# Performance work log

Measured on AMD Instinct MI355X. Metric: run time of the kernel, lower is better.

The kernel has to match this reference:

```python
import jax, jax.numpy as jnp
import numpy as np

V, E, H, L = 32000, 512, 1024, 2
B, T, S = 32, 64, 64


def setup_inputs() -> dict:
    key = jax.random.key(0)
    ks = jax.random.split(key, 20)
    sc = 0.05
    return {
        "tgt_seq": jax.random.randint(ks[0], (B, T), 0, V),
        "encoder_outputs": jax.random.normal(ks[1], (B, S, H), jnp.float32),
        "h0": jax.random.normal(ks[2], (L, B, H), jnp.float32) * sc,
        "c0": jax.random.normal(ks[3], (L, B, H), jnp.float32) * sc,
        "mask": jnp.ones((B, S), dtype=bool),
        "emb": jax.random.normal(ks[4], (V, E), jnp.float32) * sc,
        "W1": jax.random.normal(ks[5], (H, H), jnp.float32) * sc,
        "b1": jnp.zeros((H,), jnp.float32),
        "W2": jax.random.normal(ks[6], (H, H), jnp.float32) * sc,
        "b2": jnp.zeros((H,), jnp.float32),
        "v": jax.random.normal(ks[7], (H,), jnp.float32) * sc,
        "bv": jnp.zeros((), jnp.float32),
        "W_ih0": jax.random.normal(ks[8], (4 * H, E + H), jnp.float32) * sc,
        "W_hh0": jax.random.normal(ks[9], (4 * H, H), jnp.float32) * sc,
        "b_ih0": jnp.zeros((4 * H,), jnp.float32),
        "b_hh0": jnp.zeros((4 * H,), jnp.float32),
        "W_ih1": jax.random.normal(ks[10], (4 * H, H), jnp.float32) * sc,
        "W_hh1": jax.random.normal(ks[11], (4 * H, H), jnp.float32) * sc,
        "b_ih1": jnp.zeros((4 * H,), jnp.float32),
        "b_hh1": jnp.zeros((4 * H,), jnp.float32),
    }


def _lstm_cell(x, h, c, W_ih, W_hh, b_ih, b_hh):
    gates = x @ W_ih.T + b_ih + h @ W_hh.T + b_hh  # [B, 4H]
    i, f, g, o = jnp.split(gates, 4, axis=-1)      # torch gate order i,f,g,o
    c_new = jax.nn.sigmoid(f) * c + jax.nn.sigmoid(i) * jnp.tanh(g)
    h_new = jax.nn.sigmoid(o) * jnp.tanh(c_new)
    return h_new, c_new


def reference(tgt_seq, encoder_outputs, h0, c0, mask, emb, W1, b1, W2, b2, v, bv,
              W_ih0, W_hh0, b_ih0, b_hh0, W_ih1, W_hh1, b_ih1, b_hh1):
    embedded = emb[tgt_seq]                       # [B, T, E] (eval mode: dropout no-op)
    # Encoder projection for Bahdanau attention is time-invariant: precompute.
    enc_proj = encoder_outputs @ W2.T + b2        # [B, S, H]
    layer_params = [(W_ih0, W_hh0, b_ih0, b_hh0), (W_ih1, W_hh1, b_ih1, b_hh1)]

    def step(carry, emb_t):
        h, c = carry                              # each [L, B, H]
        dec_h = h[-1]                             # top-layer hidden, [B, H]
        # Bahdanau: score = v . tanh(W1 h + W2 enc)
        e = jnp.tanh((dec_h @ W1.T + b1)[:, None, :] + enc_proj)  # [B, S, H]
        scores = e @ v + bv                       # [B, S]
        scores = jnp.where(mask, scores, -1e9)
        attn = jax.nn.softmax(scores, axis=-1)
        ctx = jnp.einsum('bs,bsh->bh', attn, encoder_outputs)     # [B, H]
        x = jnp.concatenate([emb_t, ctx], axis=-1)                # [B, E+H]
        new_h, new_c = [], []
        for l in range(L):
            hl, cl = _lstm_cell(x, h[l], c[l], *layer_params[l])
            new_h.append(hl); new_c.append(cl)
            x = hl
        return (jnp.stack(new_h), jnp.stack(new_c)), x            # x = top-layer output

    (h_n, c_n), outs = jax.lax.scan(step, (h0, c0), jnp.swapaxes(embedded, 0, 1))
    decoder_outputs = jnp.swapaxes(outs, 0, 1)    # [B, T, H]
    return decoder_outputs, (h_n, c_n)
```

## Files before the change

kernel.cpp:

```cpp
#include <hip/hip_runtime.h>
#include <hip/hip_bf16.h>

#define NB 32
#define NT 64
#define NS 64
#define NH 1024
#define NE 512
#define NG 4096
#define NWG 256

typedef __attribute__((ext_vector_type(8))) short bf16x8;
typedef __attribute__((ext_vector_type(4))) float f32x4;
typedef __hip_bfloat16 bf16;

#define MFMA(a,b,c) __builtin_amdgcn_mfma_f32_16x16x32_bf16((a),(b),(c),0,0,0)

__device__ __align__(16) bf16 g_W1b  [NH*NH];
__device__ __align__(16) bf16 g_W2b  [NH*NH];
__device__ __align__(16) bf16 g_Whh0b[NG*NH];
__device__ __align__(16) bf16 g_Wih0cb[NG*NH];
__device__ __align__(16) bf16 g_Wih0eb[NG*NE];
__device__ __align__(16) bf16 g_Wih1b[NG*NH];
__device__ __align__(16) bf16 g_Whh1b[NG*NH];
__device__ __align__(16) bf16 g_encb [NB*NS*NH];
__device__ __align__(16) bf16 g_encpb[NB*NS*NH];
__device__ __align__(16) bf16 g_embtb[NT*NB*NE];
__device__ __align__(16) float g_preemb[NT*NB*NG];
__device__ __align__(16) float g_b1s[NG];
__device__ __align__(16) bf16 g_encWr[NWG*512*64];
__device__ __align__(16) bf16 g_h0buf[(NT+1)*NB*NH];
__device__ __align__(16) bf16 g_h1buf[(NT+1)*NB*NH];
__device__ __align__(16) float g_scores[NT*NB*NS];
__device__ int g_fsc[64];
__device__ int g_fh0[256];
__device__ int g_fh1[256];

__device__ __forceinline__ void st_f32(float* p, float v) {
  __hip_atomic_store(p, v, __ATOMIC_RELAXED, __HIP_MEMORY_SCOPE_AGENT);
}
__device__ __forceinline__ void st_u32(unsigned* p, unsigned v) {
  __hip_atomic_store(p, v, __ATOMIC_RELAXED, __HIP_MEMORY_SCOPE_AGENT);
}
__device__ __forceinline__ void st_i32(int* p, int v) {
  __hip_atomic_store(p, v, __ATOMIC_RELAXED, __HIP_MEMORY_SCOPE_AGENT);
}
__device__ __forceinline__ int ld_i32(const int* p) {
  return __hip_atomic_load(p, __ATOMIC_RELAXED, __HIP_MEMORY_SCOPE_AGENT);
}
__device__ __forceinline__ float ld_f32(const float* p) {
  return __hip_atomic_load(p, __ATOMIC_RELAXED, __HIP_MEMORY_SCOPE_AGENT);
}
__device__ __forceinline__ void at_addf(float* p, float v) {
  __hip_atomic_fetch_add(p, v, __ATOMIC_RELAXED, __HIP_MEMORY_SCOPE_AGENT);
}
__device__ __forceinline__ unsigned short f2bf_u(float x) {
  bf16 h = __float2bfloat16(x);
  unsigned short u; __builtin_memcpy(&u, &h, 2); return u;
}
__device__ __forceinline__ float sigm(float x)   { return 1.f / (1.f + __expf(-x)); }
__device__ __forceinline__ float tanh_f(float x) { return 1.f - 2.f / (1.f + __expf(2.f * x)); }
__device__ __forceinline__ float bf2f(short u) {
  return __uint_as_float(((unsigned)(unsigned short)u) << 16);
}

__device__ __forceinline__ void wait_flags256(const int* f, int tgt) {
  if (threadIdx.x < 64) {
    const int base = threadIdx.x * 4;
    for (;;) {
      int a = ld_i32(f + base),     b = ld_i32(f + base + 1);
      int c = ld_i32(f + base + 2), d = ld_i32(f + base + 3);
      if (__all(a >= tgt && b >= tgt && c >= tgt && d >= tgt)) break;
      __builtin_amdgcn_s_sleep(1);
    }
  }
  asm volatile("" ::: "memory");
  __syncthreads();
}
__device__ __forceinline__ void wait_flags64(const int* f, int tgt) {
  if (threadIdx.x < 64) {
    for (;;) {
      if (__all(ld_i32(f + threadIdx.x) >= tgt)) break;
      __builtin_amdgcn_s_sleep(2);
    }
  }
  asm volatile("" ::: "memory");
  __syncthreads();
}

__device__ __forceinline__ f32x4 gemm16h_lds_pf(const bf16* __restrict__ A, const bf16* Bsw,
                                                int l15, int kf8, int kh) {
  bf16x8 a[16];
  const bf16* ar = A + (size_t)l15*NH + kh*512 + kf8*8;
  #pragma unroll
  for (int k = 0; k < 16; ++k) a[k] = *(const bf16x8*)(ar + k*32);
  f32x4 acc = {0,0,0,0};
  #pragma unroll
  for (int k = 0; k < 16; ++k) {
    int bg = kh*64 + k*4 + kf8;
    acc = MFMA(a[k], *(const bf16x8*)(Bsw + (l15*128 + ((bg & ~7) | ((bg & 7) ^ (l15 & 7))))*8), acc);
  }
  return acc;
}
__device__ __forceinline__ void gemm16h_dual_pf(const bf16* __restrict__ A, const bf16* B0,
                                                const bf16* B1, int l15, int kf8, int kh,
                                                f32x4* o0, f32x4* o1) {
  bf16x8 a[16];
  const bf16* ar = A + (size_t)l15*NH + kh*512 + kf8*8;
  #pragma unroll
  for (int k = 0; k < 16; ++k) a[k] = *(const bf16x8*)(ar + k*32);
  f32x4 u = {0,0,0,0}, w = {0,0,0,0};
  #pragma unroll
  for (int k = 0; k < 16; ++k) {
    int bg = kh*64 + k*4 + kf8;
    int of = (l15*128 + ((bg & ~7) | ((bg & 7) ^ (l15 & 7))))*8;
    u = MFMA(a[k], *(const bf16x8*)(B0 + of), u);
    w = MFMA(a[k], *(const bf16x8*)(B1 + of), w);
  }
  *o0 = u; *o1 = w;
}

__global__ __launch_bounds__(256) void prep(const float* W1, const float* W2, const float* Whh0,
    const float* Wih0, const float* Wih1, const float* Whh1, const float* enc,
    const float* emb, const int* tgt) {
  long i = (long)blockIdx.x * 256 + threadIdx.x;
  if (i < 1048576) { g_W1b[i] = __float2bfloat16(W1[i]); return; } i -= 1048576;
  if (i < 1048576) { g_W2b[i] = __float2bfloat16(W2[i]); return; } i -= 1048576;
  if (i < 4194304) { g_Whh0b[i] = __float2bfloat16(Whh0[i]); return; } i -= 4194304;
  if (i < 4194304) { long r = i >> 10, c = i & 1023;
                     g_Wih0cb[i] = __float2bfloat16(Wih0[r*1536 + 512 + c]); return; } i -= 4194304;
  if (i < 2097152) { long r = i >> 9, c = i & 511;
                     g_Wih0eb[i] = __float2bfloat16(Wih0[r*1536 + c]); return; } i -= 2097152;
  if (i < 4194304) { g_Wih1b[i] = __float2bfloat16(Wih1[i]); return; } i -= 4194304;
  if (i < 4194304) { g_Whh1b[i] = __float2bfloat16(Whh1[i]); return; } i -= 4194304;
  if (i < 2097152) { g_encb[i] = __float2bfloat16(enc[i]); return; } i -= 2097152;
  { long e = i & 511, tb = i >> 9, tt = tb >> 5, b = tb & 31;
    g_embtb[i] = __float2bfloat16(emb[(long)tgt[b*NT + tt]*NE + e]); }
}

__global__ __launch_bounds__(256) void init_state(const float* h0in, const float* bih1,
                                                  const float* bhh1) {
  int i = blockIdx.x * 256 + threadIdx.x;
  if (i < NB*NH) {
    g_h0buf[i] = __float2bfloat16(h0in[i]);
    g_h1buf[i] = __float2bfloat16(h0in[NB*NH + i]);
  }
  if (i < NG) g_b1s[i] = bih1[i] + bhh1[i];
  st_f32(&g_scores[2*i], 0.f);
  st_f32(&g_scores[2*i + 1], 0.f);
  if (i < 256) { st_i32(&g_fh0[i], 0); st_i32(&g_fh1[i], 0); }
  if (i < 64) st_i32(&g_fsc[i], 0);
}

__device__ void gemm32(const bf16* __restrict__ A, const bf16* __restrict__ Bw,
                       const float* bias0, const float* bias1,
                       bf16* outB, float* outF, int M, int N, int K) {
  int gw = blockIdx.x * 4 + (threadIdx.x >> 6);
  int lane = threadIdx.x & 63;
  int nb = N >> 5;
  int mi = gw / nb, ni = gw - mi * nb;
  if (mi >= (M >> 5)) return;
  int l15 = lane & 15, lk = (lane >> 4) * 8;
  f32x4 acc00 = {0,0,0,0}, acc01 = {0,0,0,0}, acc10 = {0,0,0,0}, acc11 = {0,0,0,0};
  const bf16* a0p = A  + (size_t)(mi*32 + l15)*K + lk;
  const bf16* a1p = a0p + (size_t)16*K;
  const bf16* b0p = Bw + (size_t)(ni*32 + l15)*K + lk;
  const bf16* b1p = b0p + (size_t)16*K;
  for (int k = 0; k < K; k += 32) {
    bf16x8 a0 = *(const bf16x8*)(a0p + k);
    bf16x8 a1 = *(const bf16x8*)(a1p + k);
    bf16x8 b0 = *(const bf16x8*)(b0p + k);
    bf16x8 b1 = *(const bf16x8*)(b1p + k);
    acc00 = MFMA(a0, b0, acc00); acc01 = MFMA(a0, b1, acc01);
    acc10 = MFMA(a1, b0, acc10); acc11 = MFMA(a1, b1, acc11);
  }
  int r0 = (lane >> 4) * 4;
  #pragma unroll
  for (int nt = 0; nt < 2; ++nt) {
    int col = ni*32 + nt*16 + l15;
    float bs = (bias0 ? bias0[col] : 0.f) + (bias1 ? bias1[col] : 0.f);
    f32x4 s0 = nt ? acc01 : acc00;
    f32x4 s1 = nt ? acc11 : acc10;
    #pragma unroll
    for (int r = 0; r < 4; ++r) {
      int row0 = mi*32 + r0 + r, row1 = row0 + 16;
      float v0 = s0[r] + bs, v1 = s1[r] + bs;
      if (outB) { outB[(size_t)row0*N + col] = __float2bfloat16(v0);
                  outB[(size_t)row1*N + col] = __float2bfloat16(v1); }
      else      { outF[(size_t)row0*N + col] = v0;
                  outF[(size_t)row1*N + col] = v1; }
    }
  }
}
__global__ __launch_bounds__(256) void k_encproj(const float* b2) {
  gemm32(g_encb, g_W2b, b2, nullptr, g_encpb, nullptr, NB*NS, NH, NH);
}
__global__ __launch_bounds__(256) void k_preemb(const float* bih0, const float* bhh0) {
  gemm32(g_embtb, g_Wih0eb, bih0, bhh0, nullptr, g_preemb, NT*NB, NG, NE);
}
__global__ __launch_bounds__(256) void k_encw() {
  int gw = blockIdx.x * 4 + (threadIdx.x >> 6);
  int lane = threadIdx.x & 63;
  int mi = gw >> 7, ni = gw & 127;
  int l15 = lane & 15, lk = (lane >> 4) * 8;
  f32x4 acc00 = {0,0,0,0}, acc01 = {0,0,0,0}, acc10 = {0,0,0,0}, acc11 = {0,0,0,0};
  const bf16* a0p = g_encb + (size_t)(mi*32 + l15)*NH + lk;
  const bf16* a1p = a0p + (size_t)16*NH;
  const bf16* b0p = g_Wih0cb + (size_t)(ni*32 + l15)*NH + lk;
  const bf16* b1p = b0p + (size_t)16*NH;
  for (int k = 0; k < NH; k += 32) {
    bf16x8 a0 = *(const bf16x8*)(a0p + k);
    bf16x8 a1 = *(const bf16x8*)(a1p + k);
    bf16x8 b0 = *(const bf16x8*)(b0p + k);
    bf16x8 b1 = *(const bf16x8*)(b1p + k);
    acc00 = MFMA(a0, b0, acc00); acc01 = MFMA(a0, b1, acc01);
    acc10 = MFMA(a1, b0, acc10); acc11 = MFMA(a1, b1, acc11);
  }
  int r0 = (lane >> 4) * 4;
  #pragma unroll
  for (int nt = 0; nt < 2; ++nt) {
    int col = ni*32 + nt*16 + l15;
    int ow = (col & 1023) >> 2, lgc = ((col >> 10) << 2) | (col & 3);
    f32x4 s0 = nt ? acc01 : acc00;
    f32x4 s1 = nt ? acc11 : acc10;
    #pragma unroll
    for (int r = 0; r < 4; ++r) {
      int row0 = mi*32 + r0 + r, row1 = row0 + 16;
      int b0r = row0 >> 6, s0r = row0 & 63, b1r = row1 >> 6, s1r = row1 & 63;
      g_encWr[(((size_t)ow*32 + b0r)*16 + lgc)*64 + s0r] = __float2bfloat16(s0[r]);
      g_encWr[(((size_t)ow*32 + b1r)*16 + lgc)*64 + s1r] = __float2bfloat16(s1[r]);
    }
  }
}

__global__ __launch_bounds__(256, 1) void dec_loop(const float* __restrict__ b1,
    const float* __restrict__ v, const float* __restrict__ c0, float* __restrict__ out) {
  const int wg = blockIdx.x, tid = threadIdx.x;
  const int lane = tid & 63, wv = tid >> 6;
  const int l15 = lane & 15, kf8 = lane >> 4;
  const int mt = wv & 1, kh = wv >> 1;
  const int pr = mt*16 + kf8*4;

  __shared__ __align__(16) bf16 sw[4][16*1024];
  __shared__ float s_tmp[1024];
  __shared__ float sg0p[2][512];
  __shared__ float sg1p[512];
  __shared__ float s_dp[512];
  __shared__ float sattn[NB*64];
  __shared__ float gatesF[512];
  __shared__ float scst[2][128];

  #pragma unroll
  for (int q = 0; q < 24; ++q) {
    int gi = q*256 + tid;
    int g = gi >> 11, rem = gi & 2047;
    int gc = rem >> 7, gk = rem & 127;
    int gate = gc >> 2, hc = gc & 3;
    const bf16* src = (g == 0) ? g_Whh0b : (g == 1) ? g_Whh1b : g_Wih1b;
    bf16x8 w8 = *(const bf16x8*)(src + (size_t)(gate*NH + wg*4 + hc)*NH + gk*8);
    int gks = (gk & ~7) | ((gk & 7) ^ (gc & 7));
    *(bf16x8*)(&sw[g][(gc*128 + gks)*8]) = w8;
  }
  const bool is_dp = (wg >= 64 && wg < 128);
  const int  u = wg - 64;
  if (is_dp) {
    #pragma unroll
    for (int q = 0; q < 8; ++q) {
      int gi = q*256 + tid, gc = gi >> 7, gk = gi & 127;
      bf16x8 w8 = *(const bf16x8*)(g_W1b + (size_t)(u*16 + gc)*NH + gk*8);
      int gks = (gk & ~7) | ((gk & 7) ^ (gc & 7));
      *(bf16x8*)(&sw[3][(gc*128 + gks)*8]) = w8;
    }
  }
  if (tid < 128) {
    scst[0][tid] = c0[(size_t)(tid >> 2)*NH + wg*4 + (tid & 3)];
    scst[1][tid] = c0[(size_t)(NB + (tid >> 2))*NH + wg*4 + (tid & 3)];
  }
  __syncthreads();

  bf16x8 w0[8], w1[8];
  {
    const bf16* e0 = g_encWr + ((size_t)wg*512 + tid)*64;
    const bf16* e1 = g_encWr + ((size_t)wg*512 + 256 + tid)*64;
    #pragma unroll
    for (int i = 0; i < 8; ++i) w0[i] = *(const bf16x8*)(e0 + i*8);
    #pragma unroll
    for (int i = 0; i < 8; ++i) w1[i] = *(const bf16x8*)(e1 + i*8);
  }

  const int  gcolr = ((tid & 15) >> 2)*NH + wg*4 + (tid & 3);
  const float b1s_r = g_b1s[gcolr];
  const float dpb = is_dp ? b1[u*16 + (tid & 15)] : 0.f;
  float vr[16];
  if (is_dp) {
    #pragma unroll
    for (int c = 0; c < 16; ++c) vr[c] = v[u*16 + c];
  }
  float* out_hn = out + (size_t)NB*NT*NH;
  float* out_cn = out_hn + 2*NB*NH;

  {
    f32x4 acc = gemm16h_lds_pf(g_h0buf + (size_t)mt*16*NH, sw[0], l15, kf8, kh);
    #pragma unroll
    for (int r = 0; r < 4; ++r) sg0p[kh][(pr + r)*16 + l15] = acc[r];
  }

  for (int t = 0; t < NT; ++t) {
    const float* pe = g_preemb + (size_t)t*NB*NG;
    float pe0 = pe[(size_t)(tid >> 4)*NG + gcolr];
    float pe1 = pe[(size_t)(16 + (tid >> 4))*NG + gcolr];

    wait_flags256(g_fh1, t);
    const bf16* h1t = g_h1buf + (size_t)t*NB*NH;

    if (is_dp) {
      f32x4 aD = gemm16h_lds_pf(h1t + (size_t)mt*16*NH, sw[3], l15, kf8, kh);
      #pragma unroll
      for (int r = 0; r < 4; ++r) s_tmp[kh*512 + (pr + r)*16 + l15] = aD[r];
      __syncthreads();
      s_dp[tid]       = s_tmp[tid]       + s_tmp[512 + tid]       + dpb;
      s_dp[256 + tid] = s_tmp[256 + tid] + s_tmp[768 + tid]       + dpb;
      __syncthreads();
      {
        const int bb = tid >> 3, s0 = (tid & 7)*8;
        float dpr[16];
        #pragma unroll
        for (int c = 0; c < 16; ++c) dpr[c] = s_dp[bb*16 + c];
        #pragma unroll
        for (int k = 0; k < 8; ++k) {
          int s = s0 + ((k + u) & 7);
          const bf16* ep = g_encpb + ((size_t)(bb*NS + s))*NH + u*16;
          bf16x8 ea = *(const bf16x8*)ep;
          bf16x8 eb = *(const bf16x8*)(ep + 8);
          float p = 0.f;
          #pragma unroll
          for (int c = 0; c < 8; ++c) p += vr[c]     * tanh_f(dpr[c]     + bf2f(ea[c]));
          #pragma unroll
          for (int c = 0; c < 8; ++c) p += vr[8 + c] * tanh_f(dpr[8 + c] + bf2f(eb[c]));
          at_addf(&g_scores[(size_t)t*2048 + bb*64 + s], p);
        }
      }
      __syncthreads();
      if (tid == 0) st_i32(&g_fsc[u], t + 1);
    }

    if (wv < 2) {
      f32x4 x0 = gemm16h_lds_pf(h1t + (size_t)wv*16*NH, sw[1], l15, kf8, 0);
      f32x4 x1 = gemm16h_lds_pf(h1t + (size_t)wv*16*NH, sw[1], l15, kf8, 1);
      x0 += x1;
      #pragma unroll
      for (int r = 0; r < 4; ++r) sg1p[(wv*16 + kf8*4 + r)*16 + l15] = x0[r];
    }

    wait_flags64(g_fsc, t + 1);
    {
      const int bb = tid >> 3, s0 = (tid & 7)*8;
      float sc[8];
      #pragma unroll
      for (int k = 0; k < 8; ++k) sc[k] = ld_f32(&g_scores[(size_t)t*2048 + bb*64 + s0 + k]);
      float m = sc[0];
      #pragma unroll
      for (int k = 1; k < 8; ++k) m = fmaxf(m, sc[k]);
      #pragma unroll
      for (int o = 1; o < 8; o <<= 1) m = fmaxf(m, __shfl_xor(m, o, 64));
      float S = 0.f, e8[8];
      #pragma unroll
      for (int k = 0; k < 8; ++k) { e8[k] = __expf(sc[k] - m); S += e8[k]; }
      #pragma unroll
      for (int o = 1; o < 8; o <<= 1) S += __shfl_xor(S, o, 64);
      float invS = 1.f / S;
      #pragma unroll
      for (int k = 0; k < 8; ++k) sattn[bb*64 + s0 + k] = e8[k] * invS;
    }
    __syncthreads();
    {
      const float* at0 = sattn + (tid >> 4)*64;
      const float* at1 = sattn + (16 + (tid >> 4))*64;
      float acc0 = 0.f, acc1 = 0.f;
      #pragma unroll
      for (int i = 0; i < 8; ++i) {
        #pragma unroll
        for (int j = 0; j < 8; ++j) {
          acc0 += at0[i*8 + j] * bf2f(w0[i][j]);
          acc1 += at1[i*8 + j] * bf2f(w1[i][j]);
        }
      }
      gatesF[tid]       = acc0 + sg0p[0][tid]       + sg0p[1][tid]       + pe0;
      gatesF[256 + tid] = acc1 + sg0p[0][256 + tid] + sg0p[1][256 + tid] + pe1;
    }
    __syncthreads();
    if (tid < 128) {
      int b = tid >> 2, hc = tid & 3, col = wg*4 + hc;
      float Gi = gatesF[b*16 + hc],     Gf = gatesF[b*16 + 4 + hc];
      float Gg = gatesF[b*16 + 8 + hc], Go = gatesF[b*16 + 12 + hc];
      float ii = sigm(Gi), ff = sigm(Gf), gg = tanh_f(Gg), oo = sigm(Go);
      float c = scst[0][tid], cn = ff*c + ii*gg;
      float hn = oo * tanh_f(cn);
      scst[0][tid] = cn;
      unsigned hu = f2bf_u(hn);
      unsigned ho = __shfl_down(hu, 1, 64);
      if ((tid & 1) == 0)
        st_u32((unsigned*)(g_h0buf + (size_t)(t+1)*NB*NH + (size_t)b*NH + col), hu | (ho << 16));
      if (t == NT - 1) { out_hn[(size_t)b*NH + col] = hn; out_cn[(size_t)b*NH + col] = cn; }
    }
    __syncthreads();
    if (tid == 0) st_i32(&g_fh0[wg], t + 1);

    wait_flags256(g_fh0, t + 1);
    {
      const bf16* h0t1 = g_h0buf + (size_t)(t+1)*NB*NH;
      f32x4 aU, aV;
      gemm16h_dual_pf(h0t1 + (size_t)mt*16*NH, sw[2], sw[0], l15, kf8, kh, &aU, &aV);
      #pragma unroll
      for (int r = 0; r < 4; ++r) {
        s_tmp[kh*512 + (pr + r)*16 + l15] = aU[r];
        sg0p[kh][(pr + r)*16 + l15]       = aV[r];
      }
      __syncthreads();
      gatesF[tid]       = s_tmp[tid]       + s_tmp[512 + tid] + sg1p[tid]       + b1s_r;
      gatesF[256 + tid] = s_tmp[256 + tid] + s_tmp[768 + tid] + sg1p[256 + tid] + b1s_r;
      __syncthreads();
      if (tid < 128) {
        int b = tid >> 2, hc = tid & 3, col = wg*4 + hc;
        float Gi = gatesF[b*16 + hc],     Gf = gatesF[b*16 + 4 + hc];
        float Gg = gatesF[b*16 + 8 + hc], Go = gatesF[b*16 + 12 + hc];
        float ii = sigm(Gi), ff = sigm(Gf), gg = tanh_f(Gg), oo = sigm(Go);
        float c = scst[1][tid], cn = ff*c + ii*gg;
        float hn = oo * tanh_f(cn);
        scst[1][tid] = cn;
        unsigned hu = f2bf_u(hn);
        unsigned ho = __shfl_down(hu, 1, 64);
        if ((tid & 1) == 0)
          st_u32((unsigned*)(g_h1buf + (size_t)(t+1)*NB*NH + (size_t)b*NH + col), hu | (ho << 16));
        out[((size_t)b*NT + t)*NH + col] = hn;
        if (t == NT - 1) { out_hn[(size_t)(NB + b)*NH + col] = hn; out_cn[(size_t)(NB + b)*NH + col] = cn; }
      }
      __syncthreads();
      if (tid == 0) st_i32(&g_fh1[wg], t + 1);
    }
  }
}

extern "C" void kernel_launch(void* const* d_in, const int* in_sizes, int n_in,
                              void* d_out, int out_size, void* d_ws, size_t ws_size,
                              hipStream_t stream) {
  (void)in_sizes; (void)n_in; (void)d_ws; (void)ws_size; (void)out_size;
  const int*   tgt  = (const int*)  d_in[0];
  const float* enc  = (const float*)d_in[1];
  const float* h0   = (const float*)d_in[2];
  const float* c0   = (const float*)d_in[3];
  const float* emb  = (const float*)d_in[5];
  const float* W1   = (const float*)d_in[6];
  const float* b1   = (const float*)d_in[7];
  const float* W2   = (const float*)d_in[8];
  const float* b2   = (const float*)d_in[9];
  const float* v    = (const float*)d_in[10];
  const float* Wih0 = (const float*)d_in[12];
  const float* Whh0 = (const float*)d_in[13];
  const float* bih0 = (const float*)d_in[14];
  const float* bhh0 = (const float*)d_in[15];
  const float* Wih1 = (const float*)d_in[16];
  const float* Whh1 = (const float*)d_in[17];
  const float* bih1 = (const float*)d_in[18];
  const float* bhh1 = (const float*)d_in[19];
  float* out = (float*)d_out;

  prep<<<dim3(94208), dim3(256), 0, stream>>>(W1, W2, Whh0, Wih0, Wih1, Whh1, enc, emb, tgt);
  init_state<<<dim3(256), dim3(256), 0, stream>>>(h0, bih1, bhh1);
  k_encproj<<<dim3(512), dim3(256), 0, stream>>>(b2);
  k_preemb<<<dim3(2048), dim3(256), 0, stream>>>(bih0, bhh0);
  k_encw<<<dim3(2048), dim3(256), 0, stream>>>();
  dec_loop<<<dim3(NWG), dim3(256), 0, stream>>>(b1, v, c0, out);
}
```

Before: 2.347 ms.

## Split batch into two chunks with per-chunk flags to pipeline decoder stages

The persistent decoder loop now handles the batch as two 16-row chunks, each with its own set of global progress flags for scores, layer-0 and layer-1 hidden states. Workgroups can start a later stage on chunk 0 while other workgroups are still finishing chunk 1, which is meant to hide grid-wide barrier latency. Each warp now covers a K-quarter of a 16-row tile instead of a half of a 32-row tile, and the score wait sleeps for a shorter time. The cost is twice as many flag waits and syncthreads per step, plus a four-way reduction of partial sums through LDS.

```diff
diff --git a/kernel.cpp b/kernel.cpp
--- a/kernel.cpp
+++ b/kernel.cpp
@@ -2,6 +2,7 @@
 #include <hip/hip_bf16.h>
 
 #define NB 32
+#define NBC 16
 #define NT 64
 #define NS 64
 #define NH 1024
@@ -31,9 +32,9 @@
 __device__ __align__(16) bf16 g_h0buf[(NT+1)*NB*NH];
 __device__ __align__(16) bf16 g_h1buf[(NT+1)*NB*NH];
 __device__ __align__(16) float g_scores[NT*NB*NS];
-__device__ int g_fsc[64];
-__device__ int g_fh0[256];
-__device__ int g_fh1[256];
+__device__ int g_fsc[2][64];
+__device__ int g_fh0[2][256];
+__device__ int g_fh1[2][256];
 
 __device__ __forceinline__ void st_f32(float* p, float v) {
   __hip_atomic_store(p, v, __ATOMIC_RELAXED, __HIP_MEMORY_SCOPE_AGENT);
@@ -80,38 +81,38 @@
   if (threadIdx.x < 64) {
     for (;;) {
       if (__all(ld_i32(f + threadIdx.x) >= tgt)) break;
-      __builtin_amdgcn_s_sleep(2);
+      __builtin_amdgcn_s_sleep(1);
     }
   }
   asm volatile("" ::: "memory");
   __syncthreads();
 }
 
-__device__ __forceinline__ f32x4 gemm16h_lds_pf(const bf16* __restrict__ A, const bf16* Bsw,
-                                                int l15, int kf8, int kh) {
-  bf16x8 a[16];
-  const bf16* ar = A + (size_t)l15*NH + kh*512 + kf8*8;
-  #pragma unroll
-  for (int k = 0; k < 16; ++k) a[k] = *(const bf16x8*)(ar + k*32);
+__device__ __forceinline__ f32x4 gemm16q_pf(const bf16* __restrict__ A, const bf16* Bsw,
+                                            int l15, int kf8, int kq) {
+  bf16x8 a[8];
+  const bf16* ar = A + (size_t)l15*NH + kq*256 + kf8*8;
+  #pragma unroll
+  for (int k = 0; k < 8; ++k) a[k] = *(const bf16x8*)(ar + k*32);
   f32x4 acc = {0,0,0,0};
   #pragma unroll
-  for (int k = 0; k < 16; ++k) {
-    int bg = kh*64 + k*4 + kf8;
+  for (int k = 0; k < 8; ++k) {
+    int bg = kq*32 + k*4 + kf8;
     acc = MFMA(a[k], *(const bf16x8*)(Bsw + (l15*128 + ((bg & ~7) | ((bg & 7) ^ (l15 & 7))))*8), acc);
   }
   return acc;
 }
-__device__ __forceinline__ void gemm16h_dual_pf(const bf16* __restrict__ A, const bf16* B0,
-                                                const bf16* B1, int l15, int kf8, int kh,
+__device__ __forceinline__ void gemm16q_dual_pf(const bf16* __restrict__ A, const bf16* B0,
+                                                const bf16* B1, int l15, int kf8, int kq,
                                                 f32x4* o0, f32x4* o1) {
-  bf16x8 a[16];
-  const bf16* ar = A + (size_t)l15*NH + kh*512 + kf8*8;
-  #pragma unroll
-  for (int k = 0; k < 16; ++k) a[k] = *(const bf16x8*)(ar + k*32);
+  bf16x8 a[8];
+  const bf16* ar = A + (size_t)l15*NH + kq*256 + kf8*8;
+  #pragma unroll
+  for (int k = 0; k < 8; ++k) a[k] = *(const bf16x8*)(ar + k*32);
   f32x4 u = {0,0,0,0}, w = {0,0,0,0};
   #pragma unroll
-  for (int k = 0; k < 16; ++k) {
-    int bg = kh*64 + k*4 + kf8;
+  for (int k = 0; k < 8; ++k) {
+    int bg = kq*32 + k*4 + kf8;
     int of = (l15*128 + ((bg & ~7) | ((bg & 7) ^ (l15 & 7))))*8;
     u = MFMA(a[k], *(const bf16x8*)(B0 + of), u);
     w = MFMA(a[k], *(const bf16x8*)(B1 + of), w);
@@ -147,8 +148,9 @@
   if (i < NG) g_b1s[i] = bih1[i] + bhh1[i];
   st_f32(&g_scores[2*i], 0.f);
   st_f32(&g_scores[2*i + 1], 0.f);
-  if (i < 256) { st_i32(&g_fh0[i], 0); st_i32(&g_fh1[i], 0); }
-  if (i < 64) st_i32(&g_fsc[i], 0);
+  if (i < 256) { st_i32(&g_fh0[0][i], 0); st_i32(&g_fh0[1][i], 0);
+                 st_i32(&g_fh1[0][i], 0); st_i32(&g_fh1[1][i], 0); }
+  if (i < 64)  { st_i32(&g_fsc[0][i], 0); st_i32(&g_fsc[1][i], 0); }
 }
 
 __device__ void gemm32(const bf16* __restrict__ A, const bf16* __restrict__ Bw,
@@ -237,17 +239,17 @@
   const int wg = blockIdx.x, tid = threadIdx.x;
   const int lane = tid & 63, wv = tid >> 6;
   const int l15 = lane & 15, kf8 = lane >> 4;
-  const int mt = wv & 1, kh = wv >> 1;
-  const int pr = mt*16 + kf8*4;
+  const int kq = wv;
+  const int prb = (kf8*4)*16 + l15;
 
   __shared__ __align__(16) bf16 sw[4][16*1024];
-  __shared__ float s_tmp[1024];
-  __shared__ float sg0p[2][512];
-  __shared__ float sg1p[512];
-  __shared__ float s_dp[512];
-  __shared__ float sattn[NB*64];
-  __shared__ float gatesF[512];
-  __shared__ float scst[2][128];
+  __shared__ float sg0p[2][4][256];
+  __shared__ float sg1p[2][4][256];
+  __shared__ float sgU[4][256];
+  __shared__ float s_dp[256];
+  __shared__ float sattn[NBC*64];
+  __shared__ float gatesF[256];
+  __shared__ float scst[2][2][64];
 
   #pragma unroll
   for (int q = 0; q < 24; ++q) {
@@ -271,9 +273,12 @@
       *(bf16x8*)(&sw[3][(gc*128 + gks)*8]) = w8;
     }
   }
-  if (tid < 128) {
-    scst[0][tid] = c0[(size_t)(tid >> 2)*NH + wg*4 + (tid & 3)];
-    scst[1][tid] = c0[(size_t)(NB + (tid >> 2))*NH + wg*4 + (tid & 3)];
+  if (tid < 64) {
+    #pragma unroll
+    for (int c = 0; c < 2; ++c) {
+      scst[0][c][tid] = c0[(size_t)(c*NBC + (tid >> 2))*NH + wg*4 + (tid & 3)];
+      scst[1][c][tid] = c0[(size_t)(NB + c*NBC + (tid >> 2))*NH + wg*4 + (tid & 3)];
+    }
   }
   __syncthreads();
 
@@ -298,144 +303,150 @@
   float* out_hn = out + (size_t)NB*NT*NH;
   float* out_cn = out_hn + 2*NB*NH;
 
-  {
-    f32x4 acc = gemm16h_lds_pf(g_h0buf + (size_t)mt*16*NH, sw[0], l15, kf8, kh);
-    #pragma unroll
-    for (int r = 0; r < 4; ++r) sg0p[kh][(pr + r)*16 + l15] = acc[r];
+  #pragma unroll
+  for (int c = 0; c < 2; ++c) {
+    f32x4 acc = gemm16q_pf(g_h0buf + (size_t)c*NBC*NH, sw[0], l15, kf8, kq);
+    #pragma unroll
+    for (int r = 0; r < 4; ++r) sg0p[c][kq][prb + r*16] = acc[r];
   }
 
   for (int t = 0; t < NT; ++t) {
     const float* pe = g_preemb + (size_t)t*NB*NG;
-    float pe0 = pe[(size_t)(tid >> 4)*NG + gcolr];
-    float pe1 = pe[(size_t)(16 + (tid >> 4))*NG + gcolr];
-
-    wait_flags256(g_fh1, t);
-    const bf16* h1t = g_h1buf + (size_t)t*NB*NH;
-
-    if (is_dp) {
-      f32x4 aD = gemm16h_lds_pf(h1t + (size_t)mt*16*NH, sw[3], l15, kf8, kh);
-      #pragma unroll
-      for (int r = 0; r < 4; ++r) s_tmp[kh*512 + (pr + r)*16 + l15] = aD[r];
-      __syncthreads();
-      s_dp[tid]       = s_tmp[tid]       + s_tmp[512 + tid]       + dpb;
-      s_dp[256 + tid] = s_tmp[256 + tid] + s_tmp[768 + tid]       + dpb;
-      __syncthreads();
+    float peA = pe[(size_t)(tid >> 4)*NG + gcolr];
+    float peB = pe[(size_t)(NBC + (tid >> 4))*NG + gcolr];
+
+    #pragma unroll
+    for (int c = 0; c < 2; ++c) {
+      wait_flags256(g_fh1[c], t);
+      const bf16* h1c = g_h1buf + ((size_t)t*NB + c*NBC)*NH;
+      if (is_dp) {
+        f32x4 aD = gemm16q_pf(h1c, sw[3], l15, kf8, kq);
+        #pragma unroll
+        for (int r = 0; r < 4; ++r) sgU[kq][prb + r*16] = aD[r];
+        __syncthreads();
+        s_dp[tid] = sgU[0][tid] + sgU[1][tid] + sgU[2][tid] + sgU[3][tid] + dpb;
+        __syncthreads();
+        {
+          #pragma unroll
+          for (int k = 0; k < 4; ++k) {
+            int idx = tid*4 + k;
+            int b_l = idx >> 6, s = (idx + u) & 63;
+            const bf16* ep = g_encpb + ((size_t)((c*NBC + b_l)*NS + s))*NH + u*16;
+            bf16x8 ea = *(const bf16x8*)ep;
+            bf16x8 eb = *(const bf16x8*)(ep + 8);
+            float p = 0.f;
+            #pragma unroll
+            for (int cc = 0; cc < 8; ++cc) p += vr[cc]     * tanh_f(s_dp[b_l*16 + cc]     + bf2f(ea[cc]));
+            #pragma unroll
+            for (int cc = 0; cc < 8; ++cc) p += vr[8 + cc] * tanh_f(s_dp[b_l*16 + 8 + cc] + bf2f(eb[cc]));
+            at_addf(&g_scores[(size_t)t*2048 + (c*NBC + b_l)*64 + s], p);
+          }
+        }
+        __syncthreads();
+        if (tid == 0) st_i32(&g_fsc[c][u], t + 1);
+      }
       {
-        const int bb = tid >> 3, s0 = (tid & 7)*8;
-        float dpr[16];
-        #pragma unroll
-        for (int c = 0; c < 16; ++c) dpr[c] = s_dp[bb*16 + c];
-        #pragma unroll
-        for (int k = 0; k < 8; ++k) {
-          int s = s0 + ((k + u) & 7);
-          const bf16* ep = g_encpb + ((size_t)(bb*NS + s))*NH + u*16;
-          bf16x8 ea = *(const bf16x8*)ep;
-          bf16x8 eb = *(const bf16x8*)(ep + 8);
-          float p = 0.f;
+        f32x4 aG = gemm16q_pf(h1c, sw[1], l15, kf8, kq);
+        #pragma unroll
+        for (int r = 0; r < 4; ++r) sg1p[c][kq][prb + r*16] = aG[r];
+      }
+    }
+
+    #pragma unroll
+    for (int c = 0; c < 2; ++c) {
+      wait_flags64(g_fsc[c], t + 1);
+      {
+        const int b_l = tid >> 4, s0 = (tid & 15)*4;
+        float sc[4];
+        #pragma unroll
+        for (int k = 0; k < 4; ++k)
+          sc[k] = ld_f32(&g_scores[(size_t)t*2048 + (c*NBC + b_l)*64 + s0 + k]);
+        float m = fmaxf(fmaxf(sc[0], sc[1]), fmaxf(sc[2], sc[3]));
+        #pragma unroll
+        for (int o = 1; o < 16; o <<= 1) m = fmaxf(m, __shfl_xor(m, o, 16));
+        float S = 0.f, e4[4];
+        #pragma unroll
+        for (int k = 0; k < 4; ++k) { e4[k] = __expf(sc[k] - m); S += e4[k]; }
+        #pragma unroll
+        for (int o = 1; o < 16; o <<= 1) S += __shfl_xor(S, o, 16);
+        float invS = 1.f / S;
+        #pragma unroll
+        for (int k = 0; k < 4; ++k) sattn[b_l*64 + s0 + k] = e4[k] * invS;
+      }
+      __syncthreads();
+      {
+        const float* at = sattn + (tid >> 4)*64;
+        float acc = 0.f;
+        if (c == 0) {
           #pragma unroll
-          for (int c = 0; c < 8; ++c) p += vr[c]     * tanh_f(dpr[c]     + bf2f(ea[c]));
+          for (int i = 0; i < 8; ++i)
+            #pragma unroll
+            for (int j = 0; j < 8; ++j) acc += at[i*8 + j] * bf2f(w0[i][j]);
+        } else {
           #pragma unroll
-          for (int c = 0; c < 8; ++c) p += vr[8 + c] * tanh_f(dpr[8 + c] + bf2f(eb[c]));
-          at_addf(&g_scores[(size_t)t*2048 + bb*64 + s], p);
+          for (int i = 0; i < 8; ++i)
+            #pragma unroll
+            for (int j = 0; j < 8; ++j) acc += at[i*8 + j] * bf2f(w1[i][j]);
         }
-      }
-      __syncthreads();
-      if (tid == 0) st_i32(&g_fsc[u], t + 1);
-    }
-
-    if (wv < 2) {
-      f32x4 x0 = gemm16h_lds_pf(h1t + (size_t)wv*16*NH, sw[1], l15, kf8, 0);
-      f32x4 x1 = gemm16h_lds_pf(h1t + (size_t)wv*16*NH, sw[1], l15, kf8, 1);
-      x0 += x1;
-      #pragma unroll
-      for (int r = 0; r < 4; ++r) sg1p[(wv*16 + kf8*4 + r)*16 + l15] = x0[r];
-    }
-
-    wait_flags64(g_fsc, t + 1);
-    {
-      const int bb = tid >> 3, s0 = (tid & 7)*8;
-      float sc[8];
-      #pragma unroll
-      for (int k = 0; k < 8; ++k) sc[k] = ld_f32(&g_scores[(size_t)t*2048 + bb*64 + s0 + k]);
-      float m = sc[0];
-      #pragma unroll
-      for (int k = 1; k < 8; ++k) m = fmaxf(m, sc[k]);
-      #pragma unroll
-      for (int o = 1; o < 8; o <<= 1) m = fmaxf(m, __shfl_xor(m, o, 64));
-      float S = 0.f, e8[8];
-      #pragma unroll
-      for (int k = 0; k < 8; ++k) { e8[k] = __expf(sc[k] - m); S += e8[k]; }
-      #pragma unroll
-      for (int o = 1; o < 8; o <<= 1) S += __shfl_xor(S, o, 64);
-      float invS = 1.f / S;
-      #pragma unroll
-      for (int k = 0; k < 8; ++k) sattn[bb*64 + s0 + k] = e8[k] * invS;
-    }
-    __syncthreads();
-    {
-      const float* at0 = sattn + (tid >> 4)*64;
-      const float* at1 = sattn + (16 + (tid >> 4))*64;
-      float acc0 = 0.f, acc1 = 0.f;
-      #pragma unroll
-      for (int i = 0; i < 8; ++i) {
-        #pragma unroll
-        for (int j = 0; j < 8; ++j) {
-          acc0 += at0[i*8 + j] * bf2f(w0[i][j]);
-          acc1 += at1[i*8 + j] * bf2f(w1[i][j]);
-        }
-      }
-      gatesF[tid]       = acc0 + sg0p[0][tid]       + sg0p[1][tid]       + pe0;
-      gatesF[256 + tid] = acc1 + sg0p[0][256 + tid] + sg0p[1][256 + tid] + pe1;
-    }
-    __syncthreads();
-    if (tid < 128) {
-      int b = tid >> 2, hc = tid & 3, col = wg*4 + hc;
-      float Gi = gatesF[b*16 + hc],     Gf = gatesF[b*16 + 4 + hc];
-      float Gg = gatesF[b*16 + 8 + hc], Go = gatesF[b*16 + 12 + hc];
-      float ii = sigm(Gi), ff = sigm(Gf), gg = tanh_f(Gg), oo = sigm(Go);
-      float c = scst[0][tid], cn = ff*c + ii*gg;
-      float hn = oo * tanh_f(cn);
-      scst[0][tid] = cn;
-      unsigned hu = f2bf_u(hn);
-      unsigned ho = __shfl_down(hu, 1, 64);
-      if ((tid & 1) == 0)
-        st_u32((unsigned*)(g_h0buf + (size_t)(t+1)*NB*NH + (size_t)b*NH + col), hu | (ho << 16));
-      if (t == NT - 1) { out_hn[(size_t)b*NH + col] = hn; out_cn[(size_t)b*NH + col] = cn; }
-    }
-    __syncthreads();
-    if (tid == 0) st_i32(&g_fh0[wg], t + 1);
-
-    wait_flags256(g_fh0, t + 1);
-    {
-      const bf16* h0t1 = g_h0buf + (size_t)(t+1)*NB*NH;
-      f32x4 aU, aV;
-      gemm16h_dual_pf(h0t1 + (size_t)mt*16*NH, sw[2], sw[0], l15, kf8, kh, &aU, &aV);
-      #pragma unroll
-      for (int r = 0; r < 4; ++r) {
-        s_tmp[kh*512 + (pr + r)*16 + l15] = aU[r];
-        sg0p[kh][(pr + r)*16 + l15]       = aV[r];
-      }
-      __syncthreads();
-      gatesF[tid]       = s_tmp[tid]       + s_tmp[512 + tid] + sg1p[tid]       + b1s_r;
-      gatesF[256 + tid] = s_tmp[256 + tid] + s_tmp[768 + tid] + sg1p[256 + tid] + b1s_r;
-      __syncthreads();
-      if (tid < 128) {
-        int b = tid >> 2, hc = tid & 3, col = wg*4 + hc;
-        float Gi = gatesF[b*16 + hc],     Gf = gatesF[b*16 + 4 + hc];
-        float Gg = gatesF[b*16 + 8 + hc], Go = gatesF[b*16 + 12 + hc];
+        gatesF[tid] = acc + sg0p[c][0][tid] + sg0p[c][1][tid] + sg0p[c][2][tid] + sg0p[c][3][tid]
+                    + (c == 0 ? peA : peB);
+      }
+      __syncthreads();
+      if (tid < 64) {
+        int b_l = tid >> 2, hc = tid & 3, col = wg*4 + hc;
+        int bg = c*NBC + b_l;
+        float Gi = gatesF[b_l*16 + hc],     Gf = gatesF[b_l*16 + 4 + hc];
+        float Gg = gatesF[b_l*16 + 8 + hc], Go = gatesF[b_l*16 + 12 + hc];
         float ii = sigm(Gi), ff = sigm(Gf), gg = tanh_f(Gg), oo = sigm(Go);
-        float c = scst[1][tid], cn = ff*c + ii*gg;
+        float cc0 = scst[0][c][tid], cn = ff*cc0 + ii*gg;
         float hn = oo * tanh_f(cn);
-        scst[1][tid] = cn;
+        scst[0][c][tid] = cn;
         unsigned hu = f2bf_u(hn);
         unsigned ho = __shfl_down(hu, 1, 64);
         if ((tid & 1) == 0)
-          st_u32((unsigned*)(g_h1buf + (size_t)(t+1)*NB*NH + (size_t)b*NH + col), hu | (ho << 16));
-        out[((size_t)b*NT + t)*NH + col] = hn;
-        if (t == NT - 1) { out_hn[(size_t)(NB + b)*NH + col] = hn; out_cn[(size_t)(NB + b)*NH + col] = cn; }
-      }
-      __syncthreads();
-      if (tid == 0) st_i32(&g_fh1[wg], t + 1);
+          st_u32((unsigned*)(g_h0buf + ((size_t)(t+1)*NB + bg)*NH + col), hu | (ho << 16));
+        if (t == NT - 1) { out_hn[(size_t)bg*NH + col] = hn; out_cn[(size_t)bg*NH + col] = cn; }
+      }
+      __syncthreads();
+      if (tid == 0) st_i32(&g_fh0[c][wg], t + 1);
+    }
+
+    #pragma unroll
+    for (int c = 0; c < 2; ++c) {
+      wait_flags256(g_fh0[c], t + 1);
+      const bf16* h0c = g_h0buf + ((size_t)(t+1)*NB + c*NBC)*NH;
+      {
+        f32x4 aU, aV;
+        gemm16q_dual_pf(h0c, sw[2], sw[0], l15, kf8, kq, &aU, &aV);
+        #pragma unroll
+        for (int r = 0; r < 4; ++r) {
+          sgU[kq][prb + r*16]     = aU[r];
+          sg0p[c][kq][prb + r*16] = aV[r];
+        }
+      }
+      __syncthreads();
+      gatesF[tid] = sgU[0][tid] + sgU[1][tid] + sgU[2][tid] + sgU[3][tid]
+                  + sg1p[c][0][tid] + sg1p[c][1][tid] + sg1p[c][2][tid] + sg1p[c][3][tid] + b1s_r;
+      __syncthreads();
+      if (tid < 64) {
+        int b_l = tid >> 2, hc = tid & 3, col = wg*4 + hc;
+        int bg = c*NBC + b_l;
+        float Gi = gatesF[b_l*16 + hc],     Gf = gatesF[b_l*16 + 4 + hc];
+        float Gg = gatesF[b_l*16 + 8 + hc], Go = gatesF[b_l*16 + 12 + hc];
+        float ii = sigm(Gi), ff = sigm(Gf), gg = tanh_f(Gg), oo = sigm(Go);
+        float cc1 = scst[1][c][tid], cn = ff*cc1 + ii*gg;
+        float hn = oo * tanh_f(cn);
+        scst[1][c][tid] = cn;
+        unsigned hu = f2bf_u(hn);
+        unsigned ho = __shfl_down(hu, 1, 64);
+        if ((tid & 1) == 0)
+          st_u32((unsigned*)(g_h1buf + ((size_t)(t+1)*NB + bg)*NH + col), hu | (ho << 16));
+        out[((size_t)bg*NT + t)*NH + col] = hn;
+        if (t == NT - 1) { out_hn[(size_t)(NB + bg)*NH + col] = hn;
+                           out_cn[(size_t)(NB + bg)*NH + col] = cn; }
+      }
+      __syncthreads();
+      if (tid == 0) st_i32(&g_fh1[c][wg], t + 1);
     }
   }
 }
```

New measurement: 2.418 ms. 1.03x slower.

## Split K across four waves and wait on per-wave flag slices

Applied to the files above, without the earlier changes.

Each wave now owns a quarter of the K dimension and computes both 16-row batch tiles, sharing each LDS B-fragment load across two MFMAs. Partial sums are reduced from four LDS slices. The 256-flag wait is split so each wave only polls the 64 producer flags covering its own K range, which drops the block-wide barrier after the wait. The h1 gemm for the layer-1 input term now runs on all four waves instead of two. Attention weights reuse the same LDS scratch buffer, and the cost is more LDS partial-sum traffic and extra reduction adds.

```diff
diff --git a/kernel.cpp b/kernel.cpp
--- a/kernel.cpp
+++ b/kernel.cpp
@@ -63,60 +63,57 @@
   return __uint_as_float(((unsigned)(unsigned short)u) << 16);
 }
 
-__device__ __forceinline__ void wait_flags256(const int* f, int tgt) {
-  if (threadIdx.x < 64) {
-    const int base = threadIdx.x * 4;
-    for (;;) {
-      int a = ld_i32(f + base),     b = ld_i32(f + base + 1);
-      int c = ld_i32(f + base + 2), d = ld_i32(f + base + 3);
-      if (__all(a >= tgt && b >= tgt && c >= tgt && d >= tgt)) break;
-      __builtin_amdgcn_s_sleep(1);
-    }
+__device__ __forceinline__ void wave_wait64(const int* f, int tgt) {
+  const int i = threadIdx.x & 63;
+  for (;;) {
+    if (__all(ld_i32(f + i) >= tgt)) break;
+    __builtin_amdgcn_s_sleep(1);
   }
   asm volatile("" ::: "memory");
-  __syncthreads();
-}
-__device__ __forceinline__ void wait_flags64(const int* f, int tgt) {
-  if (threadIdx.x < 64) {
-    for (;;) {
-      if (__all(ld_i32(f + threadIdx.x) >= tgt)) break;
-      __builtin_amdgcn_s_sleep(2);
-    }
-  }
-  asm volatile("" ::: "memory");
-  __syncthreads();
-}
-
-__device__ __forceinline__ f32x4 gemm16h_lds_pf(const bf16* __restrict__ A, const bf16* Bsw,
-                                                int l15, int kf8, int kh) {
-  bf16x8 a[16];
-  const bf16* ar = A + (size_t)l15*NH + kh*512 + kf8*8;
-  #pragma unroll
-  for (int k = 0; k < 16; ++k) a[k] = *(const bf16x8*)(ar + k*32);
-  f32x4 acc = {0,0,0,0};
-  #pragma unroll
-  for (int k = 0; k < 16; ++k) {
-    int bg = kh*64 + k*4 + kf8;
-    acc = MFMA(a[k], *(const bf16x8*)(Bsw + (l15*128 + ((bg & ~7) | ((bg & 7) ^ (l15 & 7))))*8), acc);
-  }
-  return acc;
-}
-__device__ __forceinline__ void gemm16h_dual_pf(const bf16* __restrict__ A, const bf16* B0,
-                                                const bf16* B1, int l15, int kf8, int kh,
-                                                f32x4* o0, f32x4* o1) {
-  bf16x8 a[16];
-  const bf16* ar = A + (size_t)l15*NH + kh*512 + kf8*8;
-  #pragma unroll
-  for (int k = 0; k < 16; ++k) a[k] = *(const bf16x8*)(ar + k*32);
+}
+
+__device__ __forceinline__ void gemm32q_pf(const bf16* __restrict__ A, const bf16* Bsw,
+                                           int l15, int kf8, int kq, f32x4* o0, f32x4* o1) {
+  bf16x8 a0[8], a1[8];
+  const bf16* ar0 = A + (size_t)l15*NH + kq*256 + kf8*8;
+  const bf16* ar1 = ar0 + (size_t)16*NH;
+  #pragma unroll
+  for (int k = 0; k < 8; ++k) a0[k] = *(const bf16x8*)(ar0 + k*32);
+  #pragma unroll
+  for (int k = 0; k < 8; ++k) a1[k] = *(const bf16x8*)(ar1 + k*32);
   f32x4 u = {0,0,0,0}, w = {0,0,0,0};
   #pragma unroll
-  for (int k = 0; k < 16; ++k) {
-    int bg = kh*64 + k*4 + kf8;
+  for (int k = 0; k < 8; ++k) {
+    int bg = kq*32 + k*4 + kf8;
+    bf16x8 bb = *(const bf16x8*)(Bsw + (l15*128 + ((bg & ~7) | ((bg & 7) ^ (l15 & 7))))*8);
+    u = MFMA(a0[k], bb, u);
+    w = MFMA(a1[k], bb, w);
+  }
+  *o0 = u; *o1 = w;
+}
+__device__ __forceinline__ void gemm32q_dual_pf(const bf16* __restrict__ A, const bf16* B0,
+                                                const bf16* B1, int l15, int kf8, int kq,
+                                                f32x4* u0, f32x4* u1, f32x4* v0, f32x4* v1) {
+  bf16x8 a0[8], a1[8];
+  const bf16* ar0 = A + (size_t)l15*NH + kq*256 + kf8*8;
+  const bf16* ar1 = ar0 + (size_t)16*NH;
+  #pragma unroll
+  for (int k = 0; k < 8; ++k) a0[k] = *(const bf16x8*)(ar0 + k*32);
+  #pragma unroll
+  for (int k = 0; k < 8; ++k) a1[k] = *(const bf16x8*)(ar1 + k*32);
+  f32x4 p = {0,0,0,0}, q = {0,0,0,0}, r = {0,0,0,0}, s = {0,0,0,0};
+  #pragma unroll
+  for (int k = 0; k < 8; ++k) {
+    int bg = kq*32 + k*4 + kf8;
     int of = (l15*128 + ((bg & ~7) | ((bg & 7) ^ (l15 & 7))))*8;
-    u = MFMA(a[k], *(const bf16x8*)(B0 + of), u);
-    w = MFMA(a[k], *(const bf16x8*)(B1 + of), w);
-  }
-  *o0 = u; *o1 = w;
+    bf16x8 b0v = *(const bf16x8*)(B0 + of);
+    bf16x8 b1v = *(const bf16x8*)(B1 + of);
+    p = MFMA(a0[k], b0v, p);
+    q = MFMA(a1[k], b0v, q);
+    r = MFMA(a0[k], b1v, r);
+    s = MFMA(a1[k], b1v, s);
+  }
+  *u0 = p; *u1 = q; *v0 = r; *v1 = s;
 }
 
 __global__ __launch_bounds__(256) void prep(const float* W1, const float* W2, const float* Whh0,
@@ -237,15 +234,14 @@
   const int wg = blockIdx.x, tid = threadIdx.x;
   const int lane = tid & 63, wv = tid >> 6;
   const int l15 = lane & 15, kf8 = lane >> 4;
-  const int mt = wv & 1, kh = wv >> 1;
-  const int pr = mt*16 + kf8*4;
+  const int kq = wv;
+  const int prb = (kf8*4)*16 + l15;
 
   __shared__ __align__(16) bf16 sw[4][16*1024];
-  __shared__ float s_tmp[1024];
-  __shared__ float sg0p[2][512];
-  __shared__ float sg1p[512];
+  __shared__ float s_multi[2048];
+  __shared__ float sg0p[4][512];
+  __shared__ float sg1p[4][512];
   __shared__ float s_dp[512];
-  __shared__ float sattn[NB*64];
   __shared__ float gatesF[512];
   __shared__ float scst[2][128];
 
@@ -299,9 +295,13 @@
   float* out_cn = out_hn + 2*NB*NH;
 
   {
-    f32x4 acc = gemm16h_lds_pf(g_h0buf + (size_t)mt*16*NH, sw[0], l15, kf8, kh);
-    #pragma unroll
-    for (int r = 0; r < 4; ++r) sg0p[kh][(pr + r)*16 + l15] = acc[r];
+    f32x4 o0, o1;
+    gemm32q_pf(g_h0buf, sw[0], l15, kf8, kq, &o0, &o1);
+    #pragma unroll
+    for (int r = 0; r < 4; ++r) {
+      sg0p[kq][prb + r*16]       = o0[r];
+      sg0p[kq][256 + prb + r*16] = o1[r];
+    }
   }
 
   for (int t = 0; t < NT; ++t) {
@@ -309,16 +309,20 @@
     float pe0 = pe[(size_t)(tid >> 4)*NG + gcolr];
     float pe1 = pe[(size_t)(16 + (tid >> 4))*NG + gcolr];
 
-    wait_flags256(g_fh1, t);
+    wave_wait64(g_fh1 + kq*64, t);
     const bf16* h1t = g_h1buf + (size_t)t*NB*NH;
 
     if (is_dp) {
-      f32x4 aD = gemm16h_lds_pf(h1t + (size_t)mt*16*NH, sw[3], l15, kf8, kh);
-      #pragma unroll
-      for (int r = 0; r < 4; ++r) s_tmp[kh*512 + (pr + r)*16 + l15] = aD[r];
-      __syncthreads();
-      s_dp[tid]       = s_tmp[tid]       + s_tmp[512 + tid]       + dpb;
-      s_dp[256 + tid] = s_tmp[256 + tid] + s_tmp[768 + tid]       + dpb;
+      f32x4 o0, o1;
+      gemm32q_pf(h1t, sw[3], l15, kf8, kq, &o0, &o1);
+      #pragma unroll
+      for (int r = 0; r < 4; ++r) {
+        s_multi[kq*512 + prb + r*16]       = o0[r];
+        s_multi[kq*512 + 256 + prb + r*16] = o1[r];
+      }
+      __syncthreads();
+      s_dp[tid]       = s_multi[tid]       + s_multi[512 + tid]       + s_multi[1024 + tid]       + s_multi[1536 + tid]       + dpb;
+      s_dp[256 + tid] = s_multi[256 + tid] + s_multi[768 + tid]       + s_multi[1280 + tid]       + s_multi[1792 + tid]       + dpb;
       __syncthreads();
       {
         const int bb = tid >> 3, s0 = (tid & 7)*8;
@@ -343,15 +347,17 @@
       if (tid == 0) st_i32(&g_fsc[u], t + 1);
     }
 
-    if (wv < 2) {
-      f32x4 x0 = gemm16h_lds_pf(h1t + (size_t)wv*16*NH, sw[1], l15, kf8, 0);
-      f32x4 x1 = gemm16h_lds_pf(h1t + (size_t)wv*16*NH, sw[1], l15, kf8, 1);
-      x0 += x1;
-      #pragma unroll
-      for (int r = 0; r < 4; ++r) sg1p[(wv*16 + kf8*4 + r)*16 + l15] = x0[r];
-    }
-
-    wait_flags64(g_fsc, t + 1);
+    {
+      f32x4 o0, o1;
+      gemm32q_pf(h1t, sw[1], l15, kf8, kq, &o0, &o1);
+      #pragma unroll
+      for (int r = 0; r < 4; ++r) {
+        sg1p[kq][prb + r*16]       = o0[r];
+        sg1p[kq][256 + prb + r*16] = o1[r];
+      }
+    }
+
+    wave_wait64(g_fsc, t + 1);
     {
       const int bb = tid >> 3, s0 = (tid & 7)*8;
       float sc[8];
@@ -369,12 +375,12 @@
       for (int o = 1; o < 8; o <<= 1) S += __shfl_xor(S, o, 64);
       float invS = 1.f / S;
       #pragma unroll
-      for (int k = 0; k < 8; ++k) sattn[bb*64 + s0 + k] = e8[k] * invS;
+      for (int k = 0; k < 8; ++k) s_multi[bb*64 + s0 + k] = e8[k] * invS;
     }
     __syncthreads();
     {
-      const float* at0 = sattn + (tid >> 4)*64;
-      const float* at1 = sattn + (16 + (tid >> 4))*64;
+      const float* at0 = s_multi + (tid >> 4)*64;
+      const float* at1 = s_multi + (16 + (tid >> 4))*64;
       float acc0 = 0.f, acc1 = 0.f;
       #pragma unroll
       for (int i = 0; i < 8; ++i) {
@@ -384,8 +390,8 @@
           acc1 += at1[i*8 + j] * bf2f(w1[i][j]);
         }
       }
-      gatesF[tid]       = acc0 + sg0p[0][tid]       + sg0p[1][tid]       + pe0;
-      gatesF[256 + tid] = acc1 + sg0p[0][256 + tid] + sg0p[1][256 + tid] + pe1;
+      gatesF[tid]       = acc0 + sg0p[0][tid]       + sg0p[1][tid]       + sg0p[2][tid]       + sg0p[3][tid]       + pe0;
+      gatesF[256 + tid] = acc1 + sg0p[0][256 + tid] + sg0p[1][256 + tid] + sg0p[2][256 + tid] + sg0p[3][256 + tid] + pe1;
     }
     __syncthreads();
     if (tid < 128) {
@@ -405,19 +411,23 @@
     __syncthreads();
     if (tid == 0) st_i32(&g_fh0[wg], t + 1);
 
-    wait_flags256(g_fh0, t + 1);
+    wave_wait64(g_fh0 + kq*64, t + 1);
     {
       const bf16* h0t1 = g_h0buf + (size_t)(t+1)*NB*NH;
-      f32x4 aU, aV;
-      gemm16h_dual_pf(h0t1 + (size_t)mt*16*NH, sw[2], sw[0], l15, kf8, kh, &aU, &aV);
+      f32x4 u0, u1, v0, v1;
+      gemm32q_dual_pf(h0t1, sw[2], sw[0], l15, kf8, kq, &u0, &u1, &v0, &v1);
       #pragma unroll
       for (int r = 0; r < 4; ++r) {
-        s_tmp[kh*512 + (pr + r)*16 + l15] = aU[r];
-        sg0p[kh][(pr + r)*16 + l15]       = aV[r];
-      }
-      __syncthreads();
-      gatesF[tid]       = s_tmp[tid]       + s_tmp[512 + tid] + sg1p[tid]       + b1s_r;
-      gatesF[256 + tid] = s_tmp[256 + tid] + s_tmp[768 + tid] + sg1p[256 + tid] + b1s_r;
+        s_multi[kq*512 + prb + r*16]       = u0[r];
+        s_multi[kq*512 + 256 + prb + r*16] = u1[r];
+        sg0p[kq][prb + r*16]               = v0[r];
+        sg0p[kq][256 + prb + r*16]         = v1[r];
+      }
+      __syncthreads();
+      gatesF[tid]       = s_multi[tid]       + s_multi[512 + tid]       + s_multi[1024 + tid]       + s_multi[1536 + tid]
+                        + sg1p[0][tid]       + sg1p[1][tid]       + sg1p[2][tid]       + sg1p[3][tid]       + b1s_r;
+      gatesF[256 + tid] = s_multi[256 + tid] + s_multi[768 + tid]       + s_multi[1280 + tid]       + s_multi[1792 + tid]
+                        + sg1p[0][256 + tid] + sg1p[1][256 + tid] + sg1p[2][256 + tid] + sg1p[3][256 + tid] + b1s_r;
       __syncthreads();
       if (tid < 128) {
         int b = tid >> 2, hc = tid & 3, col = wg*4 + hc;
```

Measured after the change: 2.488 ms. +6.0%, slower.
